# Kernel optimization log

Measured on AMD Instinct MI355X. Metric: run time of the kernel, lower is better.

The kernel has to match this reference:

```python
import jax, jax.numpy as jnp
import numpy as np

BLOCK_H = 1
BLOCK_W = 1
EPS = 1e-6


def setup_inputs() -> dict:
    key = jax.random.key(0)
    ks = jax.random.split(key, 8)
    B, L, D = 2, 4096, 1024
    NBF, DK = 16, 64  # nb_features, d_k (d_model // n_heads)
    ws = 1.0 / np.sqrt(D)  # nn.Linear-like init scale
    return {
        "q": jax.random.normal(ks[0], (B, L, D), jnp.float32),
        "k": jax.random.normal(ks[1], (B, L, D), jnp.float32),
        "v": jax.random.normal(ks[2], (B, L, D), jnp.float32),
        "w_q": jax.random.normal(ks[3], (D, D), jnp.float32) * ws,
        "w_k": jax.random.normal(ks[4], (D, D), jnp.float32) * ws,
        "w_v": jax.random.normal(ks[5], (D, D), jnp.float32) * ws,
        "w_o": jax.random.normal(ks[6], (D, D), jnp.float32) * ws,
        "omega": jax.random.normal(ks[7], (NBF, DK), jnp.float32) / np.sqrt(DK),
    }


def reference(q, k, v, w_q, w_k, w_v, w_o, omega):
    B, Lq, D = q.shape
    Lk = k.shape[1]
    NBF, DK = omega.shape
    H = D // DK

    # projections (torch nn.Linear: x @ W.T), split into heads
    qh = (q @ w_q.T).reshape(B, Lq, H, DK)
    kh = (k @ w_k.T).reshape(B, Lk, H, DK)
    vh = (v @ w_v.T).reshape(B, Lk, H, DK)

    qp = jnp.exp(-0.5 * jnp.square(jnp.einsum('blhd,fd->blhf', qh, omega)))
    kp = jnp.exp(-0.5 * jnp.square(jnp.einsum('blhd,fd->blhf', kh, omega)))
    qp = qp / (qp.sum(-1, keepdims=True) + EPS)
    kp = kp / (kp.sum(-1, keepdims=True) + EPS)

    # causal prefix sums over key positions
    K_cum = jnp.cumsum(kp, axis=1)                                    # [B,Lk,H,F]
    KV_cum = jnp.cumsum(kp[..., None] * vh[..., None, :], axis=1)     # [B,Lk,H,F,DK]

    # blockwise causal key index per query position
    q_idx = jnp.arange(Lq)
    key_idx = jnp.clip((q_idx // BLOCK_H + 1) * BLOCK_W - 1, 0, Lk - 1)
    K_sel = K_cum[:, key_idx]      # [B,Lq,H,F]
    KV_sel = KV_cum[:, key_idx]    # [B,Lq,H,F,DK]

    numerator = jnp.einsum('blhf,blhfd->blhd', qp, KV_sel)
    denominator = jnp.sum(qp * K_sel, axis=-1, keepdims=True)
    out = (numerator / (denominator + EPS)).reshape(B, Lq, D)
    return out @ w_o.T
```

## Files before the change

### kernel.cpp

```cpp
#include <hip/hip_runtime.h>

#define L_SEQ   4096
#define BATCH   2
#define DMODEL  1024
#define HEADS   16
#define DKH     64
#define NBF     16
#define CHUNK   64
#define NCHUNK  64
#define NCHAIN  32
#define STATE_SZ 1040
#define EPSF    1e-6f

typedef __attribute__((ext_vector_type(8))) __bf16 bf16x8;
typedef __attribute__((ext_vector_type(4))) float  floatx4;

__device__ __forceinline__ unsigned short f2bf(float x) {
  unsigned u = __builtin_bit_cast(unsigned, x);
  u += 0x7fffu + ((u >> 16) & 1u);
  return (unsigned short)(u >> 16);
}
__device__ __forceinline__ float bf2f(unsigned short u) {
  return __builtin_bit_cast(float, ((unsigned)u) << 16);
}

#define GLOAD16(gp, lp) \
  __builtin_amdgcn_global_load_lds((const __attribute__((address_space(1))) void*)(gp), \
                                   (__attribute__((address_space(3))) void*)(lp), 16, 0, 0)

__global__ __launch_bounds__(256) void prep(const float* __restrict__ wv, const float* __restrict__ wo,
                                            const float* __restrict__ wq, const float* __restrict__ wk,
                                            const float* __restrict__ omega,
                                            unsigned short* __restrict__ wvb, unsigned short* __restrict__ wob,
                                            unsigned short* __restrict__ wtq, unsigned short* __restrict__ wtk) {
  __shared__ float ws[64 * 64];
  __shared__ float oms[NBF * 64];
  const int blk = blockIdx.x;
  const int tid = threadIdx.x;
  if (blk < 2048) {
    const float* in = (blk < 1024) ? wv : wo;
    unsigned short* out = (blk < 1024) ? wvb : wob;
    int i = (blk & 1023) * 256 + tid;
    float4 v4 = ((const float4*)in)[i];
    ushort4 o;
    o.x = f2bf(v4.x); o.y = f2bf(v4.y); o.z = f2bf(v4.z); o.w = f2bf(v4.w);
    ((ushort4*)out)[i] = o;
    return;
  }
  const int local = blk - 2048;
  const int z = local >> 8;
  const int h = (local & 255) >> 4;
  const int s = local & 15;
  const float* w = z ? wk : wq;
  unsigned short* wt = z ? wtk : wtq;
  for (int i = tid; i < 64 * 64; i += 256) {
    int r = i >> 6, c = i & 63;
    ws[i] = w[(size_t)(h * 64 + r) * DMODEL + s * 64 + c];
  }
  for (int i = tid; i < NBF * 64; i += 256) oms[i] = omega[i];
  __syncthreads();
  for (int j = tid; j < NBF * 64; j += 256) {
    int f = j >> 6, c = j & 63;
    float acc = 0.f;
#pragma unroll
    for (int d = 0; d < 64; ++d) acc += oms[f * 64 + d] * ws[d * 64 + c];
    wt[(size_t)(h * NBF + f) * DMODEL + s * 64 + c] = f2bf(acc);
  }
}

__global__ __launch_bounds__(256) void proj_all(const float* __restrict__ q, const float* __restrict__ k,
                                                const float* __restrict__ v,
                                                const unsigned short* __restrict__ wtq,
                                                const unsigned short* __restrict__ wtk,
                                                const unsigned short* __restrict__ wvb,
                                                float* __restrict__ qp_t, float* __restrict__ kp_t,
                                                unsigned short* __restrict__ vh) {
  constexpr int K = DMODEL, NT = K / 32;
  __shared__ char smem[2][24576];

  const int tid  = threadIdx.x;
  const int wave = tid >> 6, lane = tid & 63;

  const int bid = blockIdx.x;
  const int id = (bid & 7) * 96 + (bid >> 3);
  const int g = id / 3, r3 = id - g * 3;
  int op, mt, nt;
  const float* A;
  const unsigned short* Bt;
  if (r3 == 2) {
    op = g & 1;
    const int local = g >> 1;
    nt = (local & 1) << 7;
    mt = (local >> 1) << 7;
    A  = op ? k : q;
    Bt = op ? wtk : wtq;
  } else {
    op = 2;
    const int vt = g * 2 + r3;
    nt = (vt & 7) << 7;
    mt = (vt >> 3) << 7;
    A  = v;
    Bt = wvb;
  }

  const int wm = (wave >> 1) << 6, wn = (wave & 1) << 6;
  const int r16 = lane & 15, kg = lane >> 4;

  floatx4 acc[4][4];
#pragma unroll
  for (int m = 0; m < 4; ++m)
#pragma unroll
    for (int n = 0; n < 4; ++n) acc[m][n] = floatx4{0.f, 0.f, 0.f, 0.f};

  const int arow = wave * 32 + (lane >> 3);
  const int acolsw = ((lane & 7) ^ (lane >> 3)) << 2;
  const float* aG = A + (size_t)(mt + arow) * K + acolsw;
  const int brow = wave * 16 + (lane >> 2);
  const int bcolsw = (((lane & 3) ^ ((lane >> 3) & 3)) << 3);
  const unsigned short* bG = Bt + (size_t)(nt + brow) * K + bcolsw;

  auto stage = [&](int buf, int kt) {
    char* base = smem[buf];
#pragma unroll
    for (int j = 0; j < 4; ++j)
      GLOAD16(aG + (size_t)(8 * j) * K + kt, base + wave * 4096 + j * 1024);
    GLOAD16(bG + kt, base + 16384 + wave * 1024);
    GLOAD16(bG + (size_t)64 * K + kt, base + 16384 + 4096 + wave * 1024);
  };
  auto compute = [&](int buf) {
    const char* base = smem[buf];
    bf16x8 af[4], bfr[4];
#pragma unroll
    for (int m = 0; m < 4; ++m) {
      const int row = wm + m * 16 + r16;
      const int sA = (kg << 1) ^ (r16 & 7);
      floatx4 lo = *(const floatx4*)(base + row * 128 + sA * 16);
      floatx4 hi = *(const floatx4*)(base + row * 128 + (sA ^ 1) * 16);
#pragma unroll
      for (int t2 = 0; t2 < 4; ++t2) {
        af[m][t2]     = (__bf16)lo[t2];
        af[m][4 + t2] = (__bf16)hi[t2];
      }
    }
#pragma unroll
    for (int n = 0; n < 4; ++n) {
      const int row = wn + n * 16 + r16;
      const int sB = kg ^ ((r16 >> 1) & 3);
      bfr[n] = *(const bf16x8*)(base + 16384 + row * 64 + sB * 16);
    }
#pragma unroll
    for (int m = 0; m < 4; ++m)
#pragma unroll
      for (int n = 0; n < 4; ++n)
        acc[m][n] = __builtin_amdgcn_mfma_f32_16x16x32_bf16(af[m], bfr[n], acc[m][n], 0, 0, 0);
  };

  stage(0, 0);
  __syncthreads();
  for (int t = 0; t < NT; ++t) {
    if (t + 1 < NT) stage((t + 1) & 1, (t + 1) * 32);
    compute(t & 1);
    __syncthreads();
  }

  if (op < 2) {
    float* xp_t = op ? kp_t : qp_t;
    const int hbase = (nt + wn) >> 4;
#pragma unroll
    for (int m = 0; m < 4; ++m) {
#pragma unroll
      for (int n = 0; n < 4; ++n) {
        const int hglob = hbase + n;
#pragma unroll
        for (int r = 0; r < 4; ++r) {
          float x = acc[m][n][r];
          float p = __expf(-0.5f * x * x);
          float s = p;
          s += __shfl_xor(s, 1);
          s += __shfl_xor(s, 2);
          s += __shfl_xor(s, 4);
          s += __shfl_xor(s, 8);
          float o = p / (s + EPSF);
          const int row = mt + wm + m * 16 + kg * 4 + r;
          const int b = row >> 12, l = row & 4095;
          xp_t[(((size_t)(b * HEADS + hglob)) * L_SEQ + l) * NBF + r16] = o;
        }
      }
    }
  } else {
#pragma unroll
    for (int m = 0; m < 4; ++m) {
      const int row0 = mt + wm + m * 16 + kg * 4;
#pragma unroll
      for (int n = 0; n < 4; ++n) {
        const int col = nt + wn + n * 16 + r16;
#pragma unroll
        for (int r = 0; r < 4; ++r)
          vh[(size_t)(row0 + r) * DMODEL + col] = f2bf(acc[m][n][r]);
      }
    }
  }
}

__global__ __launch_bounds__(256) void gemm_o(const unsigned short* __restrict__ A,
                                              const unsigned short* __restrict__ Bt,
                                              float* __restrict__ C) {
  constexpr int K = DMODEL, NT = K / 32;
  __shared__ char smem[2][16384];
  const int tid  = threadIdx.x;
  const int wave = tid >> 6, lane = tid & 63;
  const int bid = blockIdx.x;
  const int id = (bid & 7) * 64 + (bid >> 3);
  const int nt = (id & 7) << 7, mt = (id >> 3) << 7;
  const int wm = (wave >> 1) << 6, wn = (wave & 1) << 6;
  const int r16 = lane & 15, kg = lane >> 4;

  floatx4 acc[4][4];
#pragma unroll
  for (int m = 0; m < 4; ++m)
#pragma unroll
    for (int n = 0; n < 4; ++n) acc[m][n] = floatx4{0.f, 0.f, 0.f, 0.f};

  const int ldrow = wave * 16 + (lane >> 2);
  const int ldcolsw = (((lane & 3) ^ ((lane >> 3) & 3)) << 3);
  const unsigned short* aG = A  + (size_t)(mt + ldrow) * K + ldcolsw;
  const unsigned short* bG = Bt + (size_t)(nt + ldrow) * K + ldcolsw;

  auto stage = [&](int buf, int kt) {
    char* base = smem[buf];
    GLOAD16(aG + kt, base + wave * 1024);
    GLOAD16(aG + (size_t)64 * K + kt, base + 4096 + wave * 1024);
    GLOAD16(bG + kt, base + 8192 + wave * 1024);
    GLOAD16(bG + (size_t)64 * K + kt, base + 8192 + 4096 + wave * 1024);
  };
  auto compute = [&](int buf) {
    const char* base = smem[buf];
    bf16x8 af[4], bfr[4];
#pragma unroll
    for (int m = 0; m < 4; ++m) {
      const int row = wm + m * 16 + r16;
      const int sA = kg ^ ((r16 >> 1) & 3);
      af[m] = *(const bf16x8*)(base + row * 64 + sA * 16);
    }
#pragma unroll
    for (int n = 0; n < 4; ++n) {
      const int row = wn + n * 16 + r16;
      const int sB = kg ^ ((r16 >> 1) & 3);
      bfr[n] = *(const bf16x8*)(base + 8192 + row * 64 + sB * 16);
    }
#pragma unroll
    for (int m = 0; m < 4; ++m)
#pragma unroll
      for (int n = 0; n < 4; ++n)
        acc[m][n] = __builtin_amdgcn_mfma_f32_16x16x32_bf16(af[m], bfr[n], acc[m][n], 0, 0, 0);
  };

  stage(0, 0);
  __syncthreads();
  for (int t = 0; t < NT; ++t) {
    if (t + 1 < NT) stage((t + 1) & 1, (t + 1) * 32);
    compute(t & 1);
    __syncthreads();
  }

#pragma unroll
  for (int m = 0; m < 4; ++m) {
    const int row0 = mt + wm + m * 16 + kg * 4;
#pragma unroll
    for (int n = 0; n < 4; ++n) {
      const int col = nt + wn + n * 16 + r16;
#pragma unroll
      for (int r = 0; r < 4; ++r)
        C[(size_t)(row0 + r) * DMODEL + col] = acc[m][n][r];
    }
  }
}

__global__ __launch_bounds__(64) void scan_chunk_sum(const float* __restrict__ kp_t,
                                                     const unsigned short* __restrict__ vh,
                                                     float* __restrict__ Sws) {
  const int c = blockIdx.x & (NCHUNK - 1);
  const int chain = blockIdx.x >> 6;
  const int b = chain >> 4, h = chain & 15;
  const int d = threadIdx.x;
  __shared__ float kp_s[CHUNK * NBF];
  const float* kpB = kp_t + ((size_t)chain * L_SEQ + c * CHUNK) * NBF;
  for (int i = 0; i < 16; ++i) kp_s[d + i * 64] = kpB[d + i * 64];
  __syncthreads();
  float S[NBF];
#pragma unroll
  for (int f = 0; f < NBF; ++f) S[f] = 0.f;
  const unsigned short* vB = vh + ((size_t)(b * L_SEQ + c * CHUNK)) * DMODEL + h * DKH + d;
  for (int l = 0; l < CHUNK; ++l) {
    float vv = bf2f(vB[(size_t)l * DMODEL]);
#pragma unroll
    for (int f = 0; f < NBF; ++f) S[f] += kp_s[l * NBF + f] * vv;
  }
  float* out = Sws + ((size_t)chain * NCHUNK + c) * STATE_SZ;
#pragma unroll
  for (int f = 0; f < NBF; ++f) out[f * 64 + d] = S[f];
  if (d < NBF) {
    float ks = 0.f;
    for (int l = 0; l < CHUNK; ++l) ks += kp_s[l * NBF + d];
    out[1024 + d] = ks;
  }
}

__global__ __launch_bounds__(64) void scan_chunks(float* __restrict__ Sws) {
  const int chain = blockIdx.x;
  const int e = blockIdx.y * 64 + threadIdx.x;
  if (e >= STATE_SZ) return;
  float acc = 0.f;
  float* p = Sws + (size_t)chain * NCHUNK * STATE_SZ + e;
  for (int c = 0; c < NCHUNK; ++c) {
    float v = p[(size_t)c * STATE_SZ];
    p[(size_t)c * STATE_SZ] = acc;
    acc += v;
  }
}

__global__ __launch_bounds__(64) void scan_apply(const float* __restrict__ qp_t,
                                                 const float* __restrict__ kp_t,
                                                 const unsigned short* __restrict__ vh,
                                                 const float* __restrict__ Sws,
                                                 unsigned short* __restrict__ attn) {
  const int c = blockIdx.x & (NCHUNK - 1);
  const int chain = blockIdx.x >> 6;
  const int b = chain >> 4, h = chain & 15;
  const int d = threadIdx.x;
  __shared__ float kp_s[CHUNK * NBF];
  __shared__ float qp_s[CHUNK * NBF];
  {
    const float* kpB = kp_t + ((size_t)chain * L_SEQ + c * CHUNK) * NBF;
    const float* qpB = qp_t + ((size_t)chain * L_SEQ + c * CHUNK) * NBF;
    for (int i = 0; i < 16; ++i) {
      kp_s[d + i * 64] = kpB[d + i * 64];
      qp_s[d + i * 64] = qpB[d + i * 64];
    }
  }
  __syncthreads();
  const float* st = Sws + ((size_t)chain * NCHUNK + c) * STATE_SZ;
  float S[NBF], kc[NBF];
#pragma unroll
  for (int f = 0; f < NBF; ++f) S[f] = st[f * 64 + d];
#pragma unroll
  for (int f = 0; f < NBF; ++f) kc[f] = st[1024 + f];
  const unsigned short* vB = vh + ((size_t)(b * L_SEQ + c * CHUNK)) * DMODEL + h * DKH + d;
  unsigned short* oB = attn + ((size_t)(b * L_SEQ + c * CHUNK)) * DMODEL + h * DKH + d;
  for (int l = 0; l < CHUNK; ++l) {
    float vv = bf2f(vB[(size_t)l * DMODEL]);
    float num = 0.f, den = 0.f;
#pragma unroll
    for (int f = 0; f < NBF; ++f) {
      float kpf = kp_s[l * NBF + f];
      S[f]  += kpf * vv;
      kc[f] += kpf;
      float qpf = qp_s[l * NBF + f];
      num += qpf * S[f];
      den += qpf * kc[f];
    }
    oB[(size_t)l * DMODEL] = f2bf(num / (den + EPSF));
  }
}

extern "C" void kernel_launch(void* const* d_in, const int* in_sizes, int n_in,
                              void* d_out, int out_size, void* d_ws, size_t ws_size,
                              hipStream_t stream) {
  const float* q   = (const float*)d_in[0];
  const float* k   = (const float*)d_in[1];
  const float* v   = (const float*)d_in[2];
  const float* w_q = (const float*)d_in[3];
  const float* w_k = (const float*)d_in[4];
  const float* w_v = (const float*)d_in[5];
  const float* w_o = (const float*)d_in[6];
  const float* omega = (const float*)d_in[7];
  float* out = (float*)d_out;

  constexpr size_t NQ = (size_t)BATCH * L_SEQ * DMODEL;
  constexpr size_t NW = (size_t)DMODEL * DMODEL;
  constexpr size_t NWT = (size_t)HEADS * NBF * DMODEL;
  constexpr size_t NP = (size_t)BATCH * HEADS * L_SEQ * NBF;
  constexpr size_t NS = (size_t)NCHAIN * NCHUNK * STATE_SZ;

  char* ws = (char*)d_ws;
  size_t off = 0;
  auto alc = [&](size_t bytes) { void* p = ws + off; off += (bytes + 255) & ~(size_t)255; return p; };
  unsigned short* wvb = (unsigned short*)alc(NW * 2);
  unsigned short* wob = (unsigned short*)alc(NW * 2);
  unsigned short* wtq = (unsigned short*)alc(NWT * 2);
  unsigned short* wtk = (unsigned short*)alc(NWT * 2);
  unsigned short* vh  = (unsigned short*)alc(NQ * 2);
  unsigned short* attn = (unsigned short*)alc(NQ * 2);
  float* qp  = (float*)alc(NP * 4);
  float* kp  = (float*)alc(NP * 4);
  float* Sws = (float*)alc(NS * 4);

  prep<<<2560, 256, 0, stream>>>(w_v, w_o, w_q, w_k, omega, wvb, wob, wtq, wtk);
  proj_all<<<768, 256, 0, stream>>>(q, k, v, wtq, wtk, wvb, qp, kp, vh);

  scan_chunk_sum<<<NCHAIN * NCHUNK, 64, 0, stream>>>(kp, vh, Sws);
  scan_chunks<<<dim3(NCHAIN, (STATE_SZ + 63) / 64), 64, 0, stream>>>(Sws);
  scan_apply<<<NCHAIN * NCHUNK, 64, 0, stream>>>(qp, kp, vh, Sws, attn);

  gemm_o<<<512, 256, 0, stream>>>(attn, wob, out);
}
```

Baseline: 145.1 us.

## Convert A tile to bf16 at staging with register prefetch pipeline in proj_all

```diff
diff --git a/kernel.cpp b/kernel.cpp
--- a/kernel.cpp
+++ b/kernel.cpp
@@ -27,6 +27,10 @@
 #define GLOAD16(gp, lp) \
   __builtin_amdgcn_global_load_lds((const __attribute__((address_space(1))) void*)(gp), \
                                    (__attribute__((address_space(3))) void*)(lp), 16, 0, 0)
+#define WAITV4L0()  asm volatile("s_waitcnt vmcnt(4) lgkmcnt(0)" ::: "memory")
+#define WAITV0L0()  asm volatile("s_waitcnt vmcnt(0) lgkmcnt(0)" ::: "memory")
+#define SBAR()      __builtin_amdgcn_s_barrier()
+#define PIN()       __builtin_amdgcn_sched_barrier(0)
 
 __global__ __launch_bounds__(256) void prep(const float* __restrict__ wv, const float* __restrict__ wo,
                                             const float* __restrict__ wq, const float* __restrict__ wk,
@@ -76,7 +80,7 @@
                                                 float* __restrict__ qp_t, float* __restrict__ kp_t,
                                                 unsigned short* __restrict__ vh) {
   constexpr int K = DMODEL, NT = K / 32;
-  __shared__ char smem[2][24576];
+  __shared__ __align__(16) char smem[2][16384];
 
   const int tid  = threadIdx.x;
   const int wave = tid >> 6, lane = tid & 63;
@@ -112,42 +116,49 @@
 #pragma unroll
     for (int n = 0; n < 4; ++n) acc[m][n] = floatx4{0.f, 0.f, 0.f, 0.f};
 
-  const int arow = wave * 32 + (lane >> 3);
-  const int acolsw = ((lane & 7) ^ (lane >> 3)) << 2;
-  const float* aG = A + (size_t)(mt + arow) * K + acolsw;
+  const int r_ = tid >> 1, hh = tid & 1;
+  const float* aG = A + (size_t)(mt + r_) * K + hh * 16;
+  const int aswz = (r_ >> 1) & 3;
+  const int awo0 = r_ * 64 + (((hh << 1) | 0) ^ aswz) * 16;
+  const int awo1 = r_ * 64 + (((hh << 1) | 1) ^ aswz) * 16;
   const int brow = wave * 16 + (lane >> 2);
   const int bcolsw = (((lane & 3) ^ ((lane >> 3) & 3)) << 3);
   const unsigned short* bG = Bt + (size_t)(nt + brow) * K + bcolsw;
 
-  auto stage = [&](int buf, int kt) {
+  float4 f0, f1, f2, f3;
+
+  auto loadA = [&](int kt) {
+    const float* p = aG + kt;
+    f0 = *(const float4*)(p);
+    f1 = *(const float4*)(p + 4);
+    f2 = *(const float4*)(p + 8);
+    f3 = *(const float4*)(p + 12);
+  };
+  auto writeA = [&](int buf) {
+    bf16x8 w0, w1;
+    w0[0] = (__bf16)f0.x; w0[1] = (__bf16)f0.y; w0[2] = (__bf16)f0.z; w0[3] = (__bf16)f0.w;
+    w0[4] = (__bf16)f1.x; w0[5] = (__bf16)f1.y; w0[6] = (__bf16)f1.z; w0[7] = (__bf16)f1.w;
+    w1[0] = (__bf16)f2.x; w1[1] = (__bf16)f2.y; w1[2] = (__bf16)f2.z; w1[3] = (__bf16)f2.w;
+    w1[4] = (__bf16)f3.x; w1[5] = (__bf16)f3.y; w1[6] = (__bf16)f3.z; w1[7] = (__bf16)f3.w;
     char* base = smem[buf];
-#pragma unroll
-    for (int j = 0; j < 4; ++j)
-      GLOAD16(aG + (size_t)(8 * j) * K + kt, base + wave * 4096 + j * 1024);
-    GLOAD16(bG + kt, base + 16384 + wave * 1024);
-    GLOAD16(bG + (size_t)64 * K + kt, base + 16384 + 4096 + wave * 1024);
+    *(bf16x8*)(base + awo0) = w0;
+    *(bf16x8*)(base + awo1) = w1;
+  };
+  auto stageB = [&](int buf, int kt) {
+    char* base = smem[buf];
+    GLOAD16(bG + kt, base + 8192 + wave * 1024);
+    GLOAD16(bG + (size_t)64 * K + kt, base + 8192 + 4096 + wave * 1024);
   };
   auto compute = [&](int buf) {
     const char* base = smem[buf];
+    const int slot = (kg ^ ((r16 >> 1) & 3)) * 16;
     bf16x8 af[4], bfr[4];
 #pragma unroll
-    for (int m = 0; m < 4; ++m) {
-      const int row = wm + m * 16 + r16;
-      const int sA = (kg << 1) ^ (r16 & 7);
-      floatx4 lo = *(const floatx4*)(base + row * 128 + sA * 16);
-      floatx4 hi = *(const floatx4*)(base + row * 128 + (sA ^ 1) * 16);
-#pragma unroll
-      for (int t2 = 0; t2 < 4; ++t2) {
-        af[m][t2]     = (__bf16)lo[t2];
-        af[m][4 + t2] = (__bf16)hi[t2];
-      }
-    }
-#pragma unroll
-    for (int n = 0; n < 4; ++n) {
-      const int row = wn + n * 16 + r16;
-      const int sB = kg ^ ((r16 >> 1) & 3);
-      bfr[n] = *(const bf16x8*)(base + 16384 + row * 64 + sB * 16);
-    }
+    for (int m = 0; m < 4; ++m)
+      af[m] = *(const bf16x8*)(base + (wm + m * 16 + r16) * 64 + slot);
+#pragma unroll
+    for (int n = 0; n < 4; ++n)
+      bfr[n] = *(const bf16x8*)(base + 8192 + (wn + n * 16 + r16) * 64 + slot);
 #pragma unroll
     for (int m = 0; m < 4; ++m)
 #pragma unroll
@@ -155,13 +166,29 @@
         acc[m][n] = __builtin_amdgcn_mfma_f32_16x16x32_bf16(af[m], bfr[n], acc[m][n], 0, 0, 0);
   };
 
-  stage(0, 0);
-  __syncthreads();
-  for (int t = 0; t < NT; ++t) {
-    if (t + 1 < NT) stage((t + 1) & 1, (t + 1) * 32);
+  loadA(0);
+  stageB(0, 0);
+  PIN();
+  writeA(0);
+  loadA(32);
+  WAITV4L0();
+  SBAR();
+
+  for (int t = 0; t < NT - 2; ++t) {
+    stageB((t + 1) & 1, (t + 1) * 32);
+    PIN();
+    writeA((t + 1) & 1);
+    loadA((t + 2) * 32);
     compute(t & 1);
-    __syncthreads();
-  }
+    WAITV4L0();
+    SBAR();
+  }
+  stageB(1, (NT - 1) * 32);
+  writeA(1);
+  compute(0);
+  WAITV0L0();
+  SBAR();
+  compute(1);
 
   if (op < 2) {
     float* xp_t = op ? kp_t : qp_t;
@@ -206,7 +233,7 @@
                                               const unsigned short* __restrict__ Bt,
                                               float* __restrict__ C) {
   constexpr int K = DMODEL, NT = K / 32;
-  __shared__ char smem[2][16384];
+  __shared__ __align__(16) char smem[2][16384];
   const int tid  = threadIdx.x;
   const int wave = tid >> 6, lane = tid & 63;
   const int bid = blockIdx.x;
@@ -235,19 +262,14 @@
   };
   auto compute = [&](int buf) {
     const char* base = smem[buf];
+    const int slot = (kg ^ ((r16 >> 1) & 3)) * 16;
     bf16x8 af[4], bfr[4];
 #pragma unroll
-    for (int m = 0; m < 4; ++m) {
-      const int row = wm + m * 16 + r16;
-      const int sA = kg ^ ((r16 >> 1) & 3);
-      af[m] = *(const bf16x8*)(base + row * 64 + sA * 16);
-    }
-#pragma unroll
-    for (int n = 0; n < 4; ++n) {
-      const int row = wn + n * 16 + r16;
-      const int sB = kg ^ ((r16 >> 1) & 3);
-      bfr[n] = *(const bf16x8*)(base + 8192 + row * 64 + sB * 16);
-    }
+    for (int m = 0; m < 4; ++m)
+      af[m] = *(const bf16x8*)(base + (wm + m * 16 + r16) * 64 + slot);
+#pragma unroll
+    for (int n = 0; n < 4; ++n)
+      bfr[n] = *(const bf16x8*)(base + 8192 + (wn + n * 16 + r16) * 64 + slot);
 #pragma unroll
     for (int m = 0; m < 4; ++m)
 #pragma unroll
```

Result: no change. 146.0 us (+0.6%).
